# Performance work log

Measured on AMD Instinct MI355X. Metric: run time of the kernel, lower is better.

Reference implementation:

```python
import jax, jax.numpy as jnp
import numpy as np

N = 2048       # x_dim (input features)
M = 2048       # y_dim (output features)
R0 = 1024      # components in table 0 (knn table)
D_K = 1024     # key encoder embed dim
D_V = 1024     # val encoder embed dim
BATCH = 512
ISTA_ALPHA = 1.0
ISTA_MAXITER = 5


def _ortho_encoder(key, n, d):
    # get_embedding_matrix with ortho=True: QR of (s,s) gaussian, take [:n,:d]
    s = max(n, d)
    q = jnp.linalg.qr(jax.random.normal(key, (s, s), dtype=jnp.float32))[0]
    return q[:n, :d]


def setup_inputs() -> dict:
    key = jax.random.key(0)
    kw, kk, kv, kx = jax.random.split(key, 4)
    W = jax.random.normal(kw, (N, M), dtype=jnp.float32) / np.float32(np.sqrt(N))
    # torch: V, S, U = svd(W); U = U.T  -> V = left vecs (n,k), U = right vecs (m,k)
    Usvd, S, Vh = jnp.linalg.svd(W, full_matrices=False)
    V = Usvd          # (n, k)
    Ur = Vh.T         # (m, k)
    key_enc = _ortho_encoder(kk, N, D_K)   # (n, d_k)
    val_enc = _ortho_encoder(kv, M, D_V)   # (m, d_v)
    # table 0: knn table over components [0:R0]
    keys_t0 = V[:, :R0].T @ key_enc        # (R0, d_k)
    vals_t0 = Ur[:, :R0].T @ val_enc       # (R0, d_v)
    scales_t0 = S[:R0][:, None]            # (R0, 1)
    # table 1: plain low-rank table over components [R0:]
    keys_t1 = V[:, R0:]                    # (n, R1)
    vals_t1 = Ur[:, R0:]                   # (m, R1)
    scales_t1 = S[R0:][:, None]            # (R1, 1)
    x = jax.random.normal(kx, (BATCH, N), dtype=jnp.float32)
    return {"x": x, "key_enc": key_enc, "val_enc": val_enc,
            "keys_t0": keys_t0, "vals_t0": vals_t0, "scales_t0": scales_t0,
            "keys_t1": keys_t1, "vals_t1": vals_t1, "scales_t1": scales_t1}


def _soft(x, t):
    return jnp.sign(x) * jnp.maximum(jnp.abs(x) - t, 0.0)


def reference(x, key_enc, val_enc, keys_t0, vals_t0, scales_t0,
              keys_t1, vals_t1, scales_t1):
    # --- table 0: knn path (batched; original looped over batch samples) ---
    q = x @ key_enc                        # (B, d_k)
    alphas = q @ keys_t0.T                 # (B, R0)
    betas = alphas * scales_t0.T           # (B, R0)
    yb = betas @ vals_t0                   # (B, d_v)
    # ISTA: min ||yb - z @ val_enc||^2 + alpha*||z||_1, step=1 (val_enc has
    # orthonormal columns so Lipschitz const of grad is 1)
    z = yb @ val_enc.T                     # z0, (B, m)
    for _ in range(ISTA_MAXITER):
        z = _soft(z + (yb - z @ val_enc) @ val_enc.T, ISTA_ALPHA)
    y = z                                  # knn path assigns y[b,:] = yh
    # --- table 1: low-rank path (accumulates) ---
    alphas2 = x @ keys_t1                  # (B, R1)
    betas2 = alphas2 * scales_t1.T         # (B, R1)
    y = y + betas2 @ vals_t1.T             # (B, m)
    return y
```

## Files before the change

### kernel.cpp

```cpp
#include <hip/hip_runtime.h>


typedef _Float16 f16x8 __attribute__((ext_vector_type(8)));
typedef _Float16 f16x4 __attribute__((ext_vector_type(4)));
typedef float f32x4 __attribute__((ext_vector_type(4)));

enum { EPI_H, EPI_QOFF, EPI_SPLIT, EPI_SOFT, EPI_ZQ, EPI_ZQF, EPI_FINAL };

typedef const __attribute__((address_space(1))) void* gas_ptr;
typedef __attribute__((address_space(3))) void* las_ptr;

__device__ __forceinline__ void gload16(const void* g, void* l) {
  __builtin_amdgcn_global_load_lds((gas_ptr)g, (las_ptr)l, 16, 0, 0);
}

__device__ __forceinline__ float softt(float t) {
  float s = fabsf(t) - 1.0f;
  s = s > 0.0f ? s : 0.0f;
  return copysignf(s, t);
}

__global__ __launch_bounds__(256) void convAll(
    const float* __restrict__ e0, const float* __restrict__ e1,
    const float* __restrict__ e2, const float* __restrict__ e3,
    _Float16* __restrict__ o0, _Float16* __restrict__ o1,
    _Float16* __restrict__ o2, _Float16* __restrict__ o3,
    const float* __restrict__ s1, const float* __restrict__ s2,
    const float4* __restrict__ pa, f16x4* __restrict__ qa, int na,
    const float4* __restrict__ pb, f16x4* __restrict__ qb, int nb,
    const float4* __restrict__ pc, f16x4* __restrict__ qc, int nc) {
  const int z = blockIdx.z;
  if (z == 4) {
    const int total = na + nb + nc;
    const int bid = blockIdx.y * 32 + blockIdx.x;
    const int nthr = 2048 * 256;
    for (int i = bid * 256 + threadIdx.y * 32 + threadIdx.x; i < total;
         i += nthr) {
      const float4* s;
      f16x4* d;
      int j = i;
      if (j < na) {
        s = pa; d = qa;
      } else if ((j -= na) < nb) {
        s = pb; d = qb;
      } else {
        j -= nb; s = pc; d = qc;
      }
      float4 v = s[j];
      f16x4 h = {(_Float16)v.x, (_Float16)v.y, (_Float16)v.z, (_Float16)v.w};
      d[j] = h;
    }
    return;
  }
  const float* in = z == 0 ? e0 : z == 1 ? e1 : z == 2 ? e2 : e3;
  _Float16* out = z == 0 ? o0 : z == 1 ? o1 : z == 2 ? o2 : o3;
  const int R = (z < 2) ? 2048 : 1024;
  const int C = 1024;
  const int mode = z == 1 ? 1 : z == 2 ? 2 : 0;
  const float* sv = z == 1 ? s1 : s2;
  __shared__ float t[32][33];
  const int tx = threadIdx.x, ty = threadIdx.y;
  const int c0 = blockIdx.x * 32, r0 = blockIdx.y * 32;
  if (r0 >= R) return;
#pragma unroll
  for (int i = 0; i < 32; i += 8)
    t[ty + i][tx] = in[(size_t)(r0 + ty + i) * C + c0 + tx];
  __syncthreads();
#pragma unroll
  for (int i = 0; i < 32; i += 8) {
    float v = t[tx][ty + i];
    if (mode == 1) v *= sv[c0 + ty + i];
    if (mode == 2) v *= sv[r0 + tx];
    out[(size_t)(c0 + ty + i) * R + r0 + tx] = (_Float16)v;
  }
}

template <int EPI>
__device__ __forceinline__ void gtile(
    const _Float16* __restrict__ A, int lda, const _Float16* __restrict__ B,
    int ldb, int nK, int N, int brow, int bcol, const float* __restrict__ dgv,
    float* __restrict__ dgout, float* __restrict__ fA, float* __restrict__ fB,
    _Float16* __restrict__ oh, _Float16* __restrict__ oh2,
    float* __restrict__ ofin, _Float16* sm, int tid) {
  const int lane = tid & 63;
  const int w = tid >> 6;
  const int wr = w & 1;
  const int wk = w >> 1;
  const int srow = lane >> 3;
  const int scol = ((lane & 7) ^ srow) << 3;
  const int a15 = lane & 15;
  const int hi = lane >> 4;
  const int l7 = lane & 7;

  const _Float16* apg = A + (size_t)(brow + (w << 4) + srow) * lda + scol;
  const _Float16* bpg = B + (size_t)(bcol + (w << 4) + srow) * ldb + scol;
  _Float16* AB = sm;
  _Float16* BB = sm + 16384;
  const int ldstA = w << 10;

  const int ca = ((wk << 2) + hi) ^ l7;
  int raddr[2], baddr[4];
#pragma unroll
  for (int mi = 0; mi < 2; ++mi)
    raddr[mi] = ((wr << 5) + (mi << 4) + a15) * 64 + (ca << 3);
#pragma unroll
  for (int ni = 0; ni < 4; ++ni)
    baddr[ni] = ((ni << 4) + a15) * 64 + (ca << 3);

  f32x4 acc[2][4] = {};

  __syncthreads();

#pragma unroll
  for (int p = 0; p < 2; ++p) {
    gload16(apg + p * 64, AB + p * 4096 + ldstA);
    gload16(apg + p * 64 + (size_t)8 * lda, AB + p * 4096 + ldstA + 512);
    gload16(bpg + p * 64, BB + p * 4096 + ldstA);
    gload16(bpg + p * 64 + (size_t)8 * ldb, BB + p * 4096 + ldstA + 512);
  }

  for (int kt = 0; kt < nK; ++kt) {
    if (kt + 2 < nK) {
      const int bf = (kt + 2) & 3;
      const int co = (kt + 2) << 6;
      gload16(apg + co, AB + bf * 4096 + ldstA);
      gload16(apg + co + (size_t)8 * lda, AB + bf * 4096 + ldstA + 512);
      gload16(bpg + co, BB + bf * 4096 + ldstA);
      gload16(bpg + co + (size_t)8 * ldb, BB + bf * 4096 + ldstA + 512);
    }
    const int rem = nK - 1 - kt;
    if (rem >= 2)
      asm volatile("s_waitcnt vmcnt(8)" ::: "memory");
    else if (rem == 1)
      asm volatile("s_waitcnt vmcnt(4)" ::: "memory");
    else
      asm volatile("s_waitcnt vmcnt(0)" ::: "memory");
    __builtin_amdgcn_s_barrier();
    __builtin_amdgcn_sched_barrier(0);
    const _Float16* Ab = AB + (kt & 3) * 4096;
    const _Float16* Bb = BB + (kt & 3) * 4096;
    f16x8 av[2], bv[4];
    av[0] = *(const f16x8*)(Ab + raddr[0]);
    av[1] = *(const f16x8*)(Ab + raddr[1]);
    bv[0] = *(const f16x8*)(Bb + baddr[0]);
    bv[1] = *(const f16x8*)(Bb + baddr[1]);
    bv[2] = *(const f16x8*)(Bb + baddr[2]);
    bv[3] = *(const f16x8*)(Bb + baddr[3]);
#pragma unroll
    for (int mi = 0; mi < 2; ++mi)
#pragma unroll
      for (int ni = 0; ni < 4; ++ni)
        acc[mi][ni] = __builtin_amdgcn_mfma_f32_16x16x32_f16(
            av[mi], bv[ni], acc[mi][ni], 0, 0, 0);
  }

  __syncthreads();
  float* scr = (float*)sm;
  const int sl = (wr << 6) + lane;
  if (wk == 1) {
#pragma unroll
    for (int mi = 0; mi < 2; ++mi)
#pragma unroll
      for (int ni = 0; ni < 4; ++ni)
#pragma unroll
        for (int r = 0; r < 4; ++r)
          scr[(((mi << 2) + ni) * 4 + r) * 128 + sl] = acc[mi][ni][r];
  }
  __syncthreads();
  if (wk == 0) {
#pragma unroll
    for (int mi = 0; mi < 2; ++mi) {
#pragma unroll
      for (int ni = 0; ni < 4; ++ni) {
#pragma unroll
        for (int r = 0; r < 4; ++r) {
          const float v =
              acc[mi][ni][r] + scr[(((mi << 2) + ni) * 4 + r) * 128 + sl];
          const int row = brow + (wr << 5) + (mi << 4) + (hi << 2) + r;
          const int col = bcol + (ni << 4) + a15;
          const size_t idx = (size_t)row * N + col;
          if constexpr (EPI == EPI_H) {
            oh[idx] = (_Float16)v;
          } else if constexpr (EPI == EPI_QOFF) {
            if (row == col) {
              dgout[row] = 1.0f - v;
              oh[idx] = (_Float16)0.0f;
            } else {
              oh[idx] = (_Float16)(-v);
            }
          } else if constexpr (EPI == EPI_SPLIT) {
            if (col < 1024)
              oh[(size_t)row * 1024 + col] = (_Float16)v;
            else
              oh2[(size_t)row * 1024 + (col - 1024)] = (_Float16)v;
          } else if constexpr (EPI == EPI_SOFT) {
            fA[idx] = v;
            float s = softt(v);
            fB[idx] = s;
            oh[idx] = (_Float16)s;
          } else if constexpr (EPI == EPI_ZQ) {
            float t = fA[idx] + dgv[col] * fB[idx] + v;
            float s = softt(t);
            fB[idx] = s;
            oh[idx] = (_Float16)s;
          } else if constexpr (EPI == EPI_ZQF) {
            float t = fA[idx] + dgv[col] * fB[idx] + v;
            fB[idx] = softt(t);
          } else {
            ofin[idx] = fB[idx] + v;
          }
        }
      }
    }
  }
}

struct WS {
  const _Float16 *ve, *vt1, *w0pT_r, *Bcat, *qoff_r, *x, *kt0s, *vt0T, *w0_r,
      *q_r, *be2;
  _Float16 *w0pT_w, *qoff_w, *w0_w, *q_w, *be2_w, *zhA, *zhB;
  float *z0, *zf, *dg;
};

__global__ __launch_bounds__(256, 2) void kD2(WS p) {
  __shared__ __align__(16) _Float16 sm[32768];
  const int tid = threadIdx.x;
  const int bid = blockIdx.x;
  if (bid < 1024) {
    gtile<EPI_QOFF>(p.ve, 1024, p.ve, 1024, 16, 2048, (bid >> 5) << 6,
                    (bid & 31) << 6, nullptr, p.dg, nullptr, nullptr, p.qoff_w,
                    nullptr, nullptr, sm, tid);
  } else if (bid < 1280) {
    const int i = bid - 1024;
    gtile<EPI_SPLIT>(p.x, 2048, p.Bcat, 2048, 32, 2048, (i >> 5) << 6,
                     (i & 31) << 6, nullptr, nullptr, nullptr, nullptr, p.q_w,
                     p.be2_w, nullptr, sm, tid);
  } else {
    const int i = bid - 1280;
    gtile<EPI_H>(p.kt0s, 1024, p.vt0T, 1024, 16, 1024, (i >> 4) << 6,
                 (i & 15) << 6, nullptr, nullptr, nullptr, nullptr, p.w0_w,
                 nullptr, nullptr, sm, tid);
  }
}

__global__ __launch_bounds__(256, 2) void kW0p(WS p) {
  __shared__ __align__(16) _Float16 sm[32768];
  const int bid = blockIdx.x;
  gtile<EPI_H>(p.ve, 1024, p.w0_r, 1024, 16, 1024, (bid >> 4) << 6,
               (bid & 15) << 6, nullptr, nullptr, nullptr, nullptr, p.w0pT_w,
               nullptr, nullptr, sm, threadIdx.x);
}

__global__ __launch_bounds__(256, 2) void kC2(WS p) {
  __shared__ __align__(16) _Float16 sm[32768];
  const int bid = blockIdx.x;
  gtile<EPI_SOFT>(p.q_r, 1024, p.w0pT_r, 1024, 16, 2048, (bid >> 5) << 6,
                  (bid & 31) << 6, nullptr, nullptr, p.z0, p.zf, p.zhA,
                  nullptr, nullptr, sm, threadIdx.x);
}

template <bool AB>
__global__ __launch_bounds__(256, 2) void kZQ(WS p) {
  __shared__ __align__(16) _Float16 sm[32768];
  const int bid = blockIdx.x;
  gtile<EPI_ZQ>(AB ? p.zhA : p.zhB, 2048, p.qoff_r, 2048, 32, 2048,
                (bid >> 5) << 6, (bid & 31) << 6, p.dg, nullptr, p.z0, p.zf,
                AB ? p.zhB : p.zhA, nullptr, nullptr, sm, threadIdx.x);
}

__global__ __launch_bounds__(256, 2) void kZQF(WS p, float* out) {
  __shared__ __align__(16) _Float16 sm[32768];
  const int bid = blockIdx.x;
  const int brow = (bid >> 5) << 6, bcol = (bid & 31) << 6;
  gtile<EPI_ZQF>(p.zhB, 2048, p.qoff_r, 2048, 32, 2048, brow, bcol, p.dg,
                 nullptr, p.z0, p.zf, nullptr, nullptr, nullptr, sm,
                 threadIdx.x);
  gtile<EPI_FINAL>(p.be2, 1024, p.vt1, 1024, 16, 2048, brow, bcol, nullptr,
                   nullptr, nullptr, p.zf, nullptr, nullptr, out, sm,
                   threadIdx.x);
}

extern "C" void kernel_launch(void* const* d_in, const int* in_sizes, int n_in,
                              void* d_out, int out_size, void* d_ws,
                              size_t ws_size, hipStream_t stream) {
  const float* x = (const float*)d_in[0];
  const float* key_enc = (const float*)d_in[1];
  const float* val_enc = (const float*)d_in[2];
  const float* keys_t0 = (const float*)d_in[3];
  const float* vals_t0 = (const float*)d_in[4];
  const float* scales_t0 = (const float*)d_in[5];
  const float* keys_t1 = (const float*)d_in[6];
  const float* vals_t1 = (const float*)d_in[7];
  const float* scales_t1 = (const float*)d_in[8];

  constexpr size_t M1 = 1048576;
  _Float16* ws = (_Float16*)d_ws;
  _Float16* ve_h = ws;
  _Float16* vt1_h = ws + 2 * M1;
  _Float16* w0pT = ws + 4 * M1;
  _Float16* Bcat = ws + 6 * M1;
  _Float16* zhA = ws + 6 * M1;
  float* z0_f = (float*)(ws + 7 * M1);
  _Float16* zhB = ws + 9 * M1;
  _Float16* qoff = ws + 10 * M1;
  _Float16* x_h = ws + 14 * M1;
  _Float16* kt0s = ws + 15 * M1;
  float* z_f = (float*)(ws + 15 * M1);
  _Float16* vt0T = ws + 16 * M1;
  _Float16* w0 = ws + 17 * M1;
  _Float16* q_h = ws + 18 * M1;
  _Float16* be2 = ws + 18 * M1 + 524288;
  float* dg = (float*)(ws + 19 * M1);

  WS p;
  p.ve = ve_h; p.vt1 = vt1_h; p.w0pT_r = w0pT; p.w0pT_w = w0pT;
  p.Bcat = Bcat; p.qoff_r = qoff; p.qoff_w = qoff; p.x = x_h;
  p.kt0s = kt0s; p.vt0T = vt0T; p.w0_r = w0; p.w0_w = w0;
  p.q_r = q_h; p.q_w = q_h; p.be2 = be2; p.be2_w = be2;
  p.zhA = zhA; p.zhB = zhB; p.z0 = z0_f; p.zf = z_f; p.dg = dg;

  convAll<<<dim3(32, 64, 5), dim3(32, 8), 0, stream>>>(
      key_enc, keys_t1, keys_t0, vals_t0, Bcat, Bcat + 2 * M1, kt0s, vt0T,
      scales_t1, scales_t0, (const float4*)x, (f16x4*)x_h, 262144,
      (const float4*)val_enc, (f16x4*)ve_h, 524288, (const float4*)vals_t1,
      (f16x4*)vt1_h, 524288);
  kD2<<<1536, 256, 0, stream>>>(p);
  kW0p<<<512, 256, 0, stream>>>(p);
  kC2<<<256, 256, 0, stream>>>(p);
  kZQ<true><<<256, 256, 0, stream>>>(p);
  kZQ<false><<<256, 256, 0, stream>>>(p);
  kZQ<true><<<256, 256, 0, stream>>>(p);
  kZQF<<<256, 256, 0, stream>>>(p, (float*)d_out);
}
```

Baseline: 120.7 us.

## Use 32x64 tiles with split-K warps for ISTA GEMMs and swizzle block mapping

Adds a new GEMM tile routine (gt32) that computes 32x64 output tiles, with four waves split across two column halves and two K halves, reduced through shared memory. The ISTA and final kernels now launch 512 blocks instead of 256, to fill more of the chip's compute units for the 512x2048 outputs. Block-index remapping groups neighbouring column tiles so blocks share operand reads in cache. In exchange there is more reduction traffic through shared memory and lower data reuse per tile.

```diff
diff --git a/kernel.cpp b/kernel.cpp
--- a/kernel.cpp
+++ b/kernel.cpp
@@ -193,7 +193,107 @@
               oh[(size_t)row * 1024 + col] = (_Float16)v;
             else
               oh2[(size_t)row * 1024 + (col - 1024)] = (_Float16)v;
-          } else if constexpr (EPI == EPI_SOFT) {
+          }
+        }
+      }
+    }
+  }
+}
+
+template <int EPI>
+__device__ __forceinline__ void gt32(
+    const _Float16* __restrict__ A, int lda, const _Float16* __restrict__ B,
+    int ldb, int nK, int N, int brow, int bcol, const float* __restrict__ dgv,
+    float* __restrict__ fA, float* __restrict__ fB,
+    _Float16* __restrict__ oh, float* __restrict__ ofin, _Float16* sm,
+    int tid) {
+  const int lane = tid & 63;
+  const int w = tid >> 6;
+  const int wc = w & 1;
+  const int wk = w >> 1;
+  const int srow = lane >> 3;
+  const int scol = ((lane & 7) ^ srow) << 3;
+  const int a15 = lane & 15, hi = lane >> 4, l7 = lane & 7;
+
+  const _Float16* apg = A + (size_t)(brow + (w << 3) + srow) * lda + scol;
+  const _Float16* bpg = B + (size_t)(bcol + (w << 4) + srow) * ldb + scol;
+  _Float16* AB = sm;
+  _Float16* BB = sm + 8192;
+  const int ca = ((wk << 2) + hi) ^ l7;
+  int raddr[2], baddr[2];
+#pragma unroll
+  for (int mi = 0; mi < 2; ++mi)
+    raddr[mi] = ((mi << 4) + a15) * 64 + (ca << 3);
+#pragma unroll
+  for (int ni = 0; ni < 2; ++ni)
+    baddr[ni] = ((wc << 5) + (ni << 4) + a15) * 64 + (ca << 3);
+
+  f32x4 acc[2][2] = {};
+  __syncthreads();
+
+#pragma unroll
+  for (int p = 0; p < 2; ++p) {
+    gload16(apg + p * 64, AB + p * 2048 + (w << 9));
+    gload16(bpg + p * 64, BB + p * 4096 + (w << 10));
+    gload16(bpg + p * 64 + (size_t)8 * ldb, BB + p * 4096 + (w << 10) + 512);
+  }
+  for (int kt = 0; kt < nK; ++kt) {
+    if (kt + 2 < nK) {
+      const int bf = (kt + 2) & 3;
+      const int co = (kt + 2) << 6;
+      gload16(apg + co, AB + bf * 2048 + (w << 9));
+      gload16(bpg + co, BB + bf * 4096 + (w << 10));
+      gload16(bpg + co + (size_t)8 * ldb, BB + bf * 4096 + (w << 10) + 512);
+    }
+    const int rem = nK - 1 - kt;
+    if (rem >= 2)
+      asm volatile("s_waitcnt vmcnt(6)" ::: "memory");
+    else if (rem == 1)
+      asm volatile("s_waitcnt vmcnt(3)" ::: "memory");
+    else
+      asm volatile("s_waitcnt vmcnt(0)" ::: "memory");
+    __builtin_amdgcn_s_barrier();
+    __builtin_amdgcn_sched_barrier(0);
+    const _Float16* Ab = AB + (kt & 3) * 2048;
+    const _Float16* Bb = BB + (kt & 3) * 4096;
+    f16x8 av[2], bv[2];
+    av[0] = *(const f16x8*)(Ab + raddr[0]);
+    av[1] = *(const f16x8*)(Ab + raddr[1]);
+    bv[0] = *(const f16x8*)(Bb + baddr[0]);
+    bv[1] = *(const f16x8*)(Bb + baddr[1]);
+#pragma unroll
+    for (int mi = 0; mi < 2; ++mi)
+#pragma unroll
+      for (int ni = 0; ni < 2; ++ni)
+        acc[mi][ni] = __builtin_amdgcn_mfma_f32_16x16x32_f16(
+            av[mi], bv[ni], acc[mi][ni], 0, 0, 0);
+  }
+  __syncthreads();
+  float* scr = (float*)sm;
+  const int sl = (wc << 6) + lane;
+  if (wk == 1) {
+#pragma unroll
+    for (int mi = 0; mi < 2; ++mi)
+#pragma unroll
+      for (int ni = 0; ni < 2; ++ni)
+#pragma unroll
+        for (int r = 0; r < 4; ++r)
+          scr[(((mi << 1) + ni) * 4 + r) * 128 + sl] = acc[mi][ni][r];
+  }
+  __syncthreads();
+  if (wk == 0) {
+#pragma unroll
+    for (int mi = 0; mi < 2; ++mi) {
+#pragma unroll
+      for (int ni = 0; ni < 2; ++ni) {
+#pragma unroll
+        for (int r = 0; r < 4; ++r) {
+          const float v =
+              acc[mi][ni][r] + scr[(((mi << 1) + ni) * 4 + r) * 128 + sl];
+          const int row = brow + (mi << 4) + (hi << 2) + r;
+          const int col = bcol + (wc << 5) + (ni << 4) + a15;
+          const size_t idx = (size_t)row * N + col;
+          if constexpr (EPI == EPI_SOFT) {
             fA[idx] = v;
             float s = softt(v);
             fB[idx] = s;
@@ -222,6 +322,12 @@
   float *z0, *zf, *dg;
 };
 
+__device__ __forceinline__ void map512(int b, int& br, int& bc) {
+  const int x = b & 7, i = b >> 3;
+  bc = (x << 2) | (i & 3);
+  br = i >> 2;
+}
+
 __global__ __launch_bounds__(256, 2) void kD2(WS p) {
   __shared__ __align__(16) _Float16 sm[32768];
   const int tid = threadIdx.x;
@@ -245,39 +351,39 @@
 
 __global__ __launch_bounds__(256, 2) void kW0p(WS p) {
   __shared__ __align__(16) _Float16 sm[32768];
-  const int bid = blockIdx.x;
-  gtile<EPI_H>(p.ve, 1024, p.w0_r, 1024, 16, 1024, (bid >> 4) << 6,
-               (bid & 15) << 6, nullptr, nullptr, nullptr, nullptr, p.w0pT_w,
-               nullptr, nullptr, sm, threadIdx.x);
+  const int x = blockIdx.x & 7, i = blockIdx.x >> 3;
+  const int bc = (x << 1) | (i & 1), br = i >> 1;
+  gtile<EPI_H>(p.ve, 1024, p.w0_r, 1024, 16, 1024, br << 6, bc << 6, nullptr,
+               nullptr, nullptr, nullptr, p.w0pT_w, nullptr, nullptr, sm,
+               threadIdx.x);
 }
 
 __global__ __launch_bounds__(256, 2) void kC2(WS p) {
-  __shared__ __align__(16) _Float16 sm[32768];
-  const int bid = blockIdx.x;
-  gtile<EPI_SOFT>(p.q_r, 1024, p.w0pT_r, 1024, 16, 2048, (bid >> 5) << 6,
-                  (bid & 31) << 6, nullptr, nullptr, p.z0, p.zf, p.zhA,
-                  nullptr, nullptr, sm, threadIdx.x);
+  __shared__ __align__(16) _Float16 sm[24576];
+  int br, bc;
+  map512(blockIdx.x, br, bc);
+  gt32<EPI_SOFT>(p.q_r, 1024, p.w0pT_r, 1024, 16, 2048, br << 5, bc << 6,
+                 nullptr, p.z0, p.zf, p.zhA, nullptr, sm, threadIdx.x);
 }
 
 template <bool AB>
 __global__ __launch_bounds__(256, 2) void kZQ(WS p) {
-  __shared__ __align__(16) _Float16 sm[32768];
-  const int bid = blockIdx.x;
-  gtile<EPI_ZQ>(AB ? p.zhA : p.zhB, 2048, p.qoff_r, 2048, 32, 2048,
-                (bid >> 5) << 6, (bid & 31) << 6, p.dg, nullptr, p.z0, p.zf,
-                AB ? p.zhB : p.zhA, nullptr, nullptr, sm, threadIdx.x);
+  __shared__ __align__(16) _Float16 sm[24576];
+  int br, bc;
+  map512(blockIdx.x, br, bc);
+  gt32<EPI_ZQ>(AB ? p.zhA : p.zhB, 2048, p.qoff_r, 2048, 32, 2048, br << 5,
+               bc << 6, p.dg, p.z0, p.zf, AB ? p.zhB : p.zhA, nullptr, sm,
+               threadIdx.x);
 }
 
 __global__ __launch_bounds__(256, 2) void kZQF(WS p, float* out) {
-  __shared__ __align__(16) _Float16 sm[32768];
-  const int bid = blockIdx.x;
-  const int brow = (bid >> 5) << 6, bcol = (bid & 31) << 6;
-  gtile<EPI_ZQF>(p.zhB, 2048, p.qoff_r, 2048, 32, 2048, brow, bcol, p.dg,
-                 nullptr, p.z0, p.zf, nullptr, nullptr, nullptr, sm,
-                 threadIdx.x);
-  gtile<EPI_FINAL>(p.be2, 1024, p.vt1, 1024, 16, 2048, brow, bcol, nullptr,
-                   nullptr, nullptr, p.zf, nullptr, nullptr, out, sm,
-                   threadIdx.x);
+  __shared__ __align__(16) _Float16 sm[24576];
+  int br, bc;
+  map512(blockIdx.x, br, bc);
+  gt32<EPI_ZQF>(p.zhB, 2048, p.qoff_r, 2048, 32, 2048, br << 5, bc << 6, p.dg,
+                p.z0, p.zf, nullptr, nullptr, sm, threadIdx.x);
+  gt32<EPI_FINAL>(p.be2, 1024, p.vt1, 1024, 16, 2048, br << 5, bc << 6,
+                  nullptr, nullptr, p.zf, nullptr, out, sm, threadIdx.x);
 }
 
 extern "C" void kernel_launch(void* const* d_in, const int* in_sizes, int n_in,
@@ -326,9 +432,9 @@
       (f16x4*)vt1_h, 524288);
   kD2<<<1536, 256, 0, stream>>>(p);
   kW0p<<<512, 256, 0, stream>>>(p);
-  kC2<<<256, 256, 0, stream>>>(p);
-  kZQ<true><<<256, 256, 0, stream>>>(p);
-  kZQ<false><<<256, 256, 0, stream>>>(p);
-  kZQ<true><<<256, 256, 0, stream>>>(p);
-  kZQF<<<256, 256, 0, stream>>>(p, (float*)d_out);
-}
+  kC2<<<512, 256, 0, stream>>>(p);
+  kZQ<true><<<512, 256, 0, stream>>>(p);
+  kZQ<false><<<512, 256, 0, stream>>>(p);
+  kZQ<true><<<512, 256, 0, stream>>>(p);
+  kZQF<<<512, 256, 0, stream>>>(p, (float*)d_out);
+}
```

Result: faster. 110.3 us (-8.7%).

## Use 32x32 split-K tiles for ISTA GEMMs, triple-buffer LDS, precompute low-rank term

Applied to the files above, without the earlier changes.

The ISTA-stage GEMMs now use 32x32 output tiles with 4-way split-K across waves. This raises block count from 256 to 1024 so more of the GPU's compute units stay busy on the batch-512 problem. LDS buffering drops from four stages to three with one tile in flight, allowing three blocks per CU. The low-rank table-1 product is computed early into a separate buffer fused into the z0 kernel launch, and the final ISTA kernel adds it in its epilogue. Block indices are remapped for L2 locality. The costs are a cross-wave LDS reduction, extra memory for the partial output, and a shallower prefetch pipeline.

```diff
diff --git a/kernel.cpp b/kernel.cpp
--- a/kernel.cpp
+++ b/kernel.cpp
@@ -5,7 +5,8 @@
 typedef _Float16 f16x4 __attribute__((ext_vector_type(4)));
 typedef float f32x4 __attribute__((ext_vector_type(4)));
 
-enum { EPI_H, EPI_QOFF, EPI_SPLIT, EPI_SOFT, EPI_ZQ, EPI_ZQF, EPI_FINAL };
+enum { EPI_H, EPI_QOFF, EPI_SPLIT };
+enum { CEPI_SOFT, CEPI_YP, CEPI_ZQ, CEPI_ZQFO };
 
 typedef const __attribute__((address_space(1))) void* gas_ptr;
 typedef __attribute__((address_space(3))) void* las_ptr;
@@ -78,10 +79,9 @@
 template <int EPI>
 __device__ __forceinline__ void gtile(
     const _Float16* __restrict__ A, int lda, const _Float16* __restrict__ B,
-    int ldb, int nK, int N, int brow, int bcol, const float* __restrict__ dgv,
-    float* __restrict__ dgout, float* __restrict__ fA, float* __restrict__ fB,
-    _Float16* __restrict__ oh, _Float16* __restrict__ oh2,
-    float* __restrict__ ofin, _Float16* sm, int tid) {
+    int ldb, int nK, int N, int brow, int bcol, float* __restrict__ dgout,
+    _Float16* __restrict__ oh, _Float16* __restrict__ oh2, _Float16* sm,
+    int tid) {
   const int lane = tid & 63;
   const int w = tid >> 6;
   const int wr = w & 1;
@@ -95,7 +95,7 @@
   const _Float16* apg = A + (size_t)(brow + (w << 4) + srow) * lda + scol;
   const _Float16* bpg = B + (size_t)(bcol + (w << 4) + srow) * ldb + scol;
   _Float16* AB = sm;
-  _Float16* BB = sm + 16384;
+  _Float16* BB = sm + 12288;
   const int ldstA = w << 10;
 
   const int ca = ((wk << 2) + hi) ^ l7;
@@ -108,37 +108,29 @@
     baddr[ni] = ((ni << 4) + a15) * 64 + (ca << 3);
 
   f32x4 acc[2][4] = {};
-
-  __syncthreads();
-
-#pragma unroll
-  for (int p = 0; p < 2; ++p) {
-    gload16(apg + p * 64, AB + p * 4096 + ldstA);
-    gload16(apg + p * 64 + (size_t)8 * lda, AB + p * 4096 + ldstA + 512);
-    gload16(bpg + p * 64, BB + p * 4096 + ldstA);
-    gload16(bpg + p * 64 + (size_t)8 * ldb, BB + p * 4096 + ldstA + 512);
-  }
-
+  __syncthreads();
+
+  gload16(apg, AB + ldstA);
+  gload16(apg + (size_t)8 * lda, AB + ldstA + 512);
+  gload16(bpg, BB + ldstA);
+  gload16(bpg + (size_t)8 * ldb, BB + ldstA + 512);
+
+  int bi = 0, bs = 1;
   for (int kt = 0; kt < nK; ++kt) {
-    if (kt + 2 < nK) {
-      const int bf = (kt + 2) & 3;
-      const int co = (kt + 2) << 6;
-      gload16(apg + co, AB + bf * 4096 + ldstA);
-      gload16(apg + co + (size_t)8 * lda, AB + bf * 4096 + ldstA + 512);
-      gload16(bpg + co, BB + bf * 4096 + ldstA);
-      gload16(bpg + co + (size_t)8 * ldb, BB + bf * 4096 + ldstA + 512);
+    if (kt + 1 < nK) {
+      const int co = (kt + 1) << 6;
+      gload16(apg + co, AB + bs * 4096 + ldstA);
+      gload16(apg + co + (size_t)8 * lda, AB + bs * 4096 + ldstA + 512);
+      gload16(bpg + co, BB + bs * 4096 + ldstA);
+      gload16(bpg + co + (size_t)8 * ldb, BB + bs * 4096 + ldstA + 512);
+      asm volatile("s_waitcnt vmcnt(4)" ::: "memory");
+    } else {
+      asm volatile("s_waitcnt vmcnt(0)" ::: "memory");
     }
-    const int rem = nK - 1 - kt;
-    if (rem >= 2)
-      asm volatile("s_waitcnt vmcnt(8)" ::: "memory");
-    else if (rem == 1)
-      asm volatile("s_waitcnt vmcnt(4)" ::: "memory");
-    else
-      asm volatile("s_waitcnt vmcnt(0)" ::: "memory");
     __builtin_amdgcn_s_barrier();
     __builtin_amdgcn_sched_barrier(0);
-    const _Float16* Ab = AB + (kt & 3) * 4096;
-    const _Float16* Bb = BB + (kt & 3) * 4096;
+    const _Float16* Ab = AB + bi * 4096;
+    const _Float16* Bb = BB + bi * 4096;
     f16x8 av[2], bv[4];
     av[0] = *(const f16x8*)(Ab + raddr[0]);
     av[1] = *(const f16x8*)(Ab + raddr[1]);
@@ -152,6 +144,8 @@
       for (int ni = 0; ni < 4; ++ni)
         acc[mi][ni] = __builtin_amdgcn_mfma_f32_16x16x32_f16(
             av[mi], bv[ni], acc[mi][ni], 0, 0, 0);
+    bi = bi == 2 ? 0 : bi + 1;
+    bs = bs == 2 ? 0 : bs + 1;
   }
 
   __syncthreads();
@@ -188,26 +182,11 @@
             } else {
               oh[idx] = (_Float16)(-v);
             }
-          } else if constexpr (EPI == EPI_SPLIT) {
+          } else {
             if (col < 1024)
               oh[(size_t)row * 1024 + col] = (_Float16)v;
             else
               oh2[(size_t)row * 1024 + (col - 1024)] = (_Float16)v;
-          } else if constexpr (EPI == EPI_SOFT) {
-            fA[idx] = v;
-            float s = softt(v);
-            fB[idx] = s;
-            oh[idx] = (_Float16)s;
-          } else if constexpr (EPI == EPI_ZQ) {
-            float t = fA[idx] + dgv[col] * fB[idx] + v;
-            float s = softt(t);
-            fB[idx] = s;
-            oh[idx] = (_Float16)s;
-          } else if constexpr (EPI == EPI_ZQF) {
-            float t = fA[idx] + dgv[col] * fB[idx] + v;
-            fB[idx] = softt(t);
-          } else {
-            ofin[idx] = fB[idx] + v;
           }
         }
       }
@@ -215,69 +194,195 @@
   }
 }
 
+template <int EPI>
+__device__ __forceinline__ void gt32k(
+    const _Float16* __restrict__ A, int lda, const _Float16* __restrict__ B,
+    int ldb, int nK, int brow, int bcol, const float* __restrict__ dgv,
+    float* __restrict__ z0f, float* __restrict__ zff, float* __restrict__ yp,
+    _Float16* __restrict__ oh, float* __restrict__ ofin, _Float16* sm,
+    int tid) {
+  const int lane = tid & 63;
+  const int w = tid >> 6;
+  const int a15 = lane & 15;
+  const int hi = lane >> 4;
+
+  const int row1 = tid >> 4;
+  const int clin = tid & 15;
+  const int scol = (clin ^ row1) << 3;
+  const _Float16* apg = A + (size_t)(brow + row1) * lda + scol;
+  const _Float16* bpg = B + (size_t)(bcol + row1) * ldb + scol;
+  _Float16* AB = sm;
+  _Float16* BB = sm + 12288;
+  const int dst = w << 9;
+
+  const int ro = ((w << 2) + hi) ^ a15;
+  const int raddr0 = a15 * 128 + (ro << 3);
+  const int raddr1 = (16 + a15) * 128 + (ro << 3);
+  const int baddr0 = raddr0;
+  const int baddr1 = raddr1;
+
+  f32x4 acc[2][2] = {};
+  __syncthreads();
+
+  gload16(apg, AB + dst);
+  gload16(apg + (size_t)16 * lda, AB + dst + 2048);
+  gload16(bpg, BB + dst);
+  gload16(bpg + (size_t)16 * ldb, BB + dst + 2048);
+
+  int bi = 0, bs = 1;
+  for (int kt = 0; kt < nK; ++kt) {
+    if (kt + 1 < nK) {
+      const int co = (kt + 1) << 7;
+      gload16(apg + co, AB + bs * 4096 + dst);
+      gload16(apg + co + (size_t)16 * lda, AB + bs * 4096 + dst + 2048);
+      gload16(bpg + co, BB + bs * 4096 + dst);
+      gload16(bpg + co + (size_t)16 * ldb, BB + bs * 4096 + dst + 2048);
+      asm volatile("s_waitcnt vmcnt(4)" ::: "memory");
+    } else {
+      asm volatile("s_waitcnt vmcnt(0)" ::: "memory");
+    }
+    __builtin_amdgcn_s_barrier();
+    __builtin_amdgcn_sched_barrier(0);
+    const _Float16* Ab = AB + bi * 4096;
+    const _Float16* Bb = BB + bi * 4096;
+    f16x8 av0 = *(const f16x8*)(Ab + raddr0);
+    f16x8 av1 = *(const f16x8*)(Ab + raddr1);
+    f16x8 bv0 = *(const f16x8*)(Bb + baddr0);
+    f16x8 bv1 = *(const f16x8*)(Bb + baddr1);
+    acc[0][0] =
+        __builtin_amdgcn_mfma_f32_16x16x32_f16(av0, bv0, acc[0][0], 0, 0, 0);
+    acc[0][1] =
+        __builtin_amdgcn_mfma_f32_16x16x32_f16(av0, bv1, acc[0][1], 0, 0, 0);
+    acc[1][0] =
+        __builtin_amdgcn_mfma_f32_16x16x32_f16(av1, bv0, acc[1][0], 0, 0, 0);
+    acc[1][1] =
+        __builtin_amdgcn_mfma_f32_16x16x32_f16(av1, bv1, acc[1][1], 0, 0, 0);
+    bi = bi == 2 ? 0 : bi + 1;
+    bs = bs == 2 ? 0 : bs + 1;
+  }
+
+  __syncthreads();
+  float* scr = (float*)sm;
+  if (w) {
+#pragma unroll
+    for (int mi = 0; mi < 2; ++mi)
+#pragma unroll
+      for (int ni = 0; ni < 2; ++ni)
+#pragma unroll
+        for (int r = 0; r < 4; ++r)
+          scr[((((w - 1) << 2) + (mi << 1) + ni) * 4 + r) * 64 + lane] =
+              acc[mi][ni][r];
+  }
+  __syncthreads();
+  if (w != 0) return;
+#pragma unroll
+  for (int mi = 0; mi < 2; ++mi) {
+#pragma unroll
+    for (int ni = 0; ni < 2; ++ni) {
+#pragma unroll
+      for (int j = 0; j < 3; ++j)
+#pragma unroll
+        for (int r = 0; r < 4; ++r)
+          acc[mi][ni][r] +=
+              scr[(((j << 2) + (mi << 1) + ni) * 4 + r) * 64 + lane];
+#pragma unroll
+      for (int r = 0; r < 4; ++r) {
+        const int row = brow + (mi << 4) + (hi << 2) + r;
+        const int col = bcol + (ni << 4) + a15;
+        const float v = acc[mi][ni][r];
+        const size_t idx = (size_t)row * 2048 + col;
+        if constexpr (EPI == CEPI_SOFT) {
+          z0f[idx] = v;
+          float s = softt(v);
+          zff[idx] = s;
+          oh[idx] = (_Float16)s;
+        } else if constexpr (EPI == CEPI_YP) {
+          yp[idx] = v;
+        } else if constexpr (EPI == CEPI_ZQ) {
+          float t = z0f[idx] + dgv[col] * zff[idx] + v;
+          float s = softt(t);
+          zff[idx] = s;
+          oh[idx] = (_Float16)s;
+        } else {
+          float t = z0f[idx] + dgv[col] * zff[idx] + v;
+          ofin[idx] = yp[idx] + softt(t);
+        }
+      }
+    }
+  }
+}
+
 struct WS {
   const _Float16 *ve, *vt1, *w0pT_r, *Bcat, *qoff_r, *x, *kt0s, *vt0T, *w0_r,
       *q_r, *be2;
   _Float16 *w0pT_w, *qoff_w, *w0_w, *q_w, *be2_w, *zhA, *zhB;
-  float *z0, *zf, *dg;
+  float *z0, *zf, *dg, *yp;
 };
 
-__global__ __launch_bounds__(256, 2) void kD2(WS p) {
-  __shared__ __align__(16) _Float16 sm[32768];
+__device__ __forceinline__ void mapc(int b, int& br, int& bc) {
+  const int x = b & 7, i = b >> 3;
+  bc = (x << 3) | (i & 7);
+  br = i >> 3;
+}
+
+__global__ __launch_bounds__(256, 3) void kD2(WS p) {
+  __shared__ __align__(16) _Float16 sm[24576];
   const int tid = threadIdx.x;
   const int bid = blockIdx.x;
   if (bid < 1024) {
     gtile<EPI_QOFF>(p.ve, 1024, p.ve, 1024, 16, 2048, (bid >> 5) << 6,
-                    (bid & 31) << 6, nullptr, p.dg, nullptr, nullptr, p.qoff_w,
-                    nullptr, nullptr, sm, tid);
+                    (bid & 31) << 6, p.dg, p.qoff_w, nullptr, sm, tid);
   } else if (bid < 1280) {
     const int i = bid - 1024;
     gtile<EPI_SPLIT>(p.x, 2048, p.Bcat, 2048, 32, 2048, (i >> 5) << 6,
-                     (i & 31) << 6, nullptr, nullptr, nullptr, nullptr, p.q_w,
-                     p.be2_w, nullptr, sm, tid);
+                     (i & 31) << 6, nullptr, p.q_w, p.be2_w, sm, tid);
   } else {
     const int i = bid - 1280;
     gtile<EPI_H>(p.kt0s, 1024, p.vt0T, 1024, 16, 1024, (i >> 4) << 6,
-                 (i & 15) << 6, nullptr, nullptr, nullptr, nullptr, p.w0_w,
-                 nullptr, nullptr, sm, tid);
-  }
-}
-
-__global__ __launch_bounds__(256, 2) void kW0p(WS p) {
-  __shared__ __align__(16) _Float16 sm[32768];
+                 (i & 15) << 6, nullptr, p.w0_w, nullptr, sm, tid);
+  }
+}
+
+__global__ __launch_bounds__(256, 3) void kW0p(WS p) {
+  __shared__ __align__(16) _Float16 sm[24576];
+  const int x = blockIdx.x & 7, i = blockIdx.x >> 3;
+  const int bc = (x << 1) | (i & 1), br = i >> 1;
+  gtile<EPI_H>(p.ve, 1024, p.w0_r, 1024, 16, 1024, br << 6, bc << 6, nullptr,
+               p.w0pT_w, nullptr, sm, threadIdx.x);
+}
+
+__global__ __launch_bounds__(256, 3) void kD4(WS p) {
+  __shared__ __align__(16) _Float16 sm[24576];
   const int bid = blockIdx.x;
-  gtile<EPI_H>(p.ve, 1024, p.w0_r, 1024, 16, 1024, (bid >> 4) << 6,
-               (bid & 15) << 6, nullptr, nullptr, nullptr, nullptr, p.w0pT_w,
-               nullptr, nullptr, sm, threadIdx.x);
-}
-
-__global__ __launch_bounds__(256, 2) void kC2(WS p) {
-  __shared__ __align__(16) _Float16 sm[32768];
-  const int bid = blockIdx.x;
-  gtile<EPI_SOFT>(p.q_r, 1024, p.w0pT_r, 1024, 16, 2048, (bid >> 5) << 6,
-                  (bid & 31) << 6, nullptr, nullptr, p.z0, p.zf, p.zhA,
-                  nullptr, nullptr, sm, threadIdx.x);
+  int br, bc;
+  if (bid < 1024) {
+    mapc(bid, br, bc);
+    gt32k<CEPI_SOFT>(p.q_r, 1024, p.w0pT_r, 1024, 8, br << 5, bc << 5,
+                     nullptr, p.z0, p.zf, nullptr, p.zhA, nullptr, sm,
+                     threadIdx.x);
+  } else {
+    mapc(bid - 1024, br, bc);
+    gt32k<CEPI_YP>(p.be2, 1024, p.vt1, 1024, 8, br << 5, bc << 5, nullptr,
+                   nullptr, nullptr, p.yp, nullptr, nullptr, sm, threadIdx.x);
+  }
 }
 
 template <bool AB>
-__global__ __launch_bounds__(256, 2) void kZQ(WS p) {
-  __shared__ __align__(16) _Float16 sm[32768];
-  const int bid = blockIdx.x;
-  gtile<EPI_ZQ>(AB ? p.zhA : p.zhB, 2048, p.qoff_r, 2048, 32, 2048,
-                (bid >> 5) << 6, (bid & 31) << 6, p.dg, nullptr, p.z0, p.zf,
-                AB ? p.zhB : p.zhA, nullptr, nullptr, sm, threadIdx.x);
-}
-
-__global__ __launch_bounds__(256, 2) void kZQF(WS p, float* out) {
-  __shared__ __align__(16) _Float16 sm[32768];
-  const int bid = blockIdx.x;
-  const int brow = (bid >> 5) << 6, bcol = (bid & 31) << 6;
-  gtile<EPI_ZQF>(p.zhB, 2048, p.qoff_r, 2048, 32, 2048, brow, bcol, p.dg,
-                 nullptr, p.z0, p.zf, nullptr, nullptr, nullptr, sm,
-                 threadIdx.x);
-  gtile<EPI_FINAL>(p.be2, 1024, p.vt1, 1024, 16, 2048, brow, bcol, nullptr,
-                   nullptr, nullptr, p.zf, nullptr, nullptr, out, sm,
-                   threadIdx.x);
+__global__ __launch_bounds__(256, 3) void kZQ(WS p) {
+  __shared__ __align__(16) _Float16 sm[24576];
+  int br, bc;
+  mapc(blockIdx.x, br, bc);
+  gt32k<CEPI_ZQ>(AB ? p.zhA : p.zhB, 2048, p.qoff_r, 2048, 16, br << 5,
+                 bc << 5, p.dg, p.z0, p.zf, nullptr, AB ? p.zhB : p.zhA,
+                 nullptr, sm, threadIdx.x);
+}
+
+__global__ __launch_bounds__(256, 3) void kZQF(WS p, float* out) {
+  __shared__ __align__(16) _Float16 sm[24576];
+  int br, bc;
+  mapc(blockIdx.x, br, bc);
+  gt32k<CEPI_ZQFO>(p.zhB, 2048, p.qoff_r, 2048, 16, br << 5, bc << 5, p.dg,
+                   p.z0, p.zf, p.yp, nullptr, out, sm, threadIdx.x);
 }
 
 extern "C" void kernel_launch(void* const* d_in, const int* in_sizes, int n_in,
@@ -311,13 +416,14 @@
   _Float16* q_h = ws + 18 * M1;
   _Float16* be2 = ws + 18 * M1 + 524288;
   float* dg = (float*)(ws + 19 * M1);
+  float* yp = (float*)(ws + 20 * M1);
 
   WS p;
   p.ve = ve_h; p.vt1 = vt1_h; p.w0pT_r = w0pT; p.w0pT_w = w0pT;
   p.Bcat = Bcat; p.qoff_r = qoff; p.qoff_w = qoff; p.x = x_h;
   p.kt0s = kt0s; p.vt0T = vt0T; p.w0_r = w0; p.w0_w = w0;
   p.q_r = q_h; p.q_w = q_h; p.be2 = be2; p.be2_w = be2;
-  p.zhA = zhA; p.zhB = zhB; p.z0 = z0_f; p.zf = z_f; p.dg = dg;
+  p.zhA = zhA; p.zhB = zhB; p.z0 = z0_f; p.zf = z_f; p.dg = dg; p.yp = yp;
 
   convAll<<<dim3(32, 64, 5), dim3(32, 8), 0, stream>>>(
       key_enc, keys_t1, keys_t0, vals_t0, Bcat, Bcat + 2 * M1, kt0s, vt0T,
@@ -326,9 +432,9 @@
       (f16x4*)vt1_h, 524288);
   kD2<<<1536, 256, 0, stream>>>(p);
   kW0p<<<512, 256, 0, stream>>>(p);
-  kC2<<<256, 256, 0, stream>>>(p);
-  kZQ<true><<<256, 256, 0, stream>>>(p);
-  kZQ<false><<<256, 256, 0, stream>>>(p);
-  kZQ<true><<<256, 256, 0, stream>>>(p);
-  kZQF<<<256, 256, 0, stream>>>(p, (float*)d_out);
-}
+  kD4<<<2048, 256, 0, stream>>>(p);
+  kZQ<true><<<1024, 256, 0, stream>>>(p);
+  kZQ<false><<<1024, 256, 0, stream>>>(p);
+  kZQ<true><<<1024, 256, 0, stream>>>(p);
+  kZQF<<<1024, 256, 0, stream>>>(p, (float*)d_out);
+}
```

After: 125.9 us. 1.04x slower.
